# Kernel optimization log

Measured on AMD Instinct MI355X. Metric: run time of the kernel, lower is better.

## Reference

```python
import jax, jax.numpy as jnp
import numpy as np

DIM = 256
HEADS = 8
WIN = 8
HIDDEN = 1024
EPS = 1e-5

def _rel_pos_index(w):
    coords = np.stack(np.meshgrid(np.arange(w), np.arange(w), indexing='ij'))  # [2,w,w]
    cf = coords.reshape(2, -1)
    rel = cf[:, :, None] - cf[:, None, :]  # [2,N,N]
    rel = rel.transpose(1, 2, 0)
    rel[:, :, 0] += w - 1
    rel[:, :, 1] += w - 1
    rel[:, :, 0] *= 2 * w - 1
    return jnp.asarray(rel.sum(-1))  # [N,N] int

REL_IDX = _rel_pos_index(WIN)

def _layernorm(x, g, b):
    mu = jnp.mean(x, -1, keepdims=True)
    var = jnp.mean(jnp.square(x - mu), -1, keepdims=True)
    return (x - mu) * jax.lax.rsqrt(var + EPS) * g + b

def setup_inputs() -> dict:
    key = jax.random.key(0)
    ks = jax.random.split(key, 12)
    s = 0.02
    return {
        'x': jax.random.normal(ks[0], (16, 4096, 256), jnp.float32),
        'H': 64,
        'W': 64,
        'ln1_g': jnp.ones((DIM,), jnp.float32),
        'ln1_b': jnp.zeros((DIM,), jnp.float32),
        'qkv_w': jax.random.normal(ks[1], (DIM, 3 * DIM), jnp.float32) * s,
        'proj_w': jax.random.normal(ks[2], (DIM, DIM), jnp.float32) * s,
        'proj_b': jnp.zeros((DIM,), jnp.float32),
        'rel_bias_table': jax.random.normal(ks[3], ((2 * WIN - 1) ** 2, HEADS), jnp.float32) * s,
        'ln2_g': jnp.ones((DIM,), jnp.float32),
        'ln2_b': jnp.zeros((DIM,), jnp.float32),
        'fc1_w': jax.random.normal(ks[4], (DIM, HIDDEN), jnp.float32) * s,
        'fc1_b': jnp.zeros((HIDDEN,), jnp.float32),
        'fc2_w': jax.random.normal(ks[5], (HIDDEN, DIM), jnp.float32) * s,
        'fc2_b': jnp.zeros((DIM,), jnp.float32),
    }

def reference(x, H, W, ln1_g, ln1_b, qkv_w, proj_w, proj_b, rel_bias_table,
              ln2_g, ln2_b, fc1_w, fc1_b, fc2_w, fc2_b):
    B, L, C = x.shape
    w = WIN
    N = w * w
    head_dim = C // HEADS
    scale = head_dim ** -0.5

    shortcut = x
    h = _layernorm(x, ln1_g, ln1_b).reshape(B, H, W, C)
    # H, W chosen divisible by window_size -> pad_h = pad_w = 0 (faithful fast path)
    # window partition: [B*nW, N, C]
    h = h.reshape(B, H // w, w, W // w, w, C).transpose(0, 1, 3, 2, 4, 5)
    xw = h.reshape(-1, N, C)
    Bw = xw.shape[0]

    qkv = (xw @ qkv_w).reshape(Bw, N, 3, HEADS, head_dim)
    q = qkv[:, :, 0].transpose(0, 2, 1, 3) * scale  # [Bw,h,N,d]
    k = qkv[:, :, 1].transpose(0, 2, 1, 3)
    v = qkv[:, :, 2].transpose(0, 2, 1, 3)

    attn = jnp.einsum('bhnd,bhmd->bhnm', q, k)
    bias = rel_bias_table[REL_IDX.reshape(-1)].reshape(N, N, HEADS).transpose(2, 0, 1)
    attn = jax.nn.softmax(attn + bias[None], axis=-1)
    out = jnp.einsum('bhnm,bhmd->bhnd', attn, v).transpose(0, 2, 1, 3).reshape(Bw, N, C)
    out = out @ proj_w + proj_b

    # window reverse
    out = out.reshape(B, H // w, W // w, w, w, C).transpose(0, 1, 3, 2, 4, 5)
    out = out.reshape(B, L, C)

    x = shortcut + out
    h2 = _layernorm(x, ln2_g, ln2_b)
    mlp = jax.nn.gelu(h2 @ fc1_w + fc1_b, approximate=False) @ fc2_w + fc2_b
    return x + mlp
```

## Files before the change

### kernel.cpp

```cpp
#include <hip/hip_runtime.h>
#include <hip/hip_bf16.h>

typedef __attribute__((ext_vector_type(8))) short bf16x8;
typedef __attribute__((ext_vector_type(4))) float f32x4;

typedef __attribute__((address_space(3))) void LdsVoid;
typedef const __attribute__((address_space(1))) void GblVoid;

__device__ __forceinline__ void gload16(const void* g, void* l) {
  __builtin_amdgcn_global_load_lds((GblVoid*)g, (LdsVoid*)l, 16, 0, 0);
}

__device__ __forceinline__ unsigned short f2bf(float f) {
  union { float f; unsigned int u; } x; x.f = f;
  unsigned int r = (x.u + 0x7fffu + ((x.u >> 16) & 1u)) >> 16;
  return (unsigned short)r;
}

__device__ __forceinline__ unsigned int cvt_pk_bf16(float a, float b) {
  unsigned int r;
  asm("v_cvt_pk_bf16_f32 %0, %1, %2" : "=v"(r) : "v"(a), "v"(b));
  return r;
}

__device__ __forceinline__ float gelu_f(float t) {
  float u = t * (0.7978845608028654f + 0.03567740814f * t * t);
  float e = __expf(2.0f * u);
  float th = 1.0f - 2.0f * __builtin_amdgcn_rcpf(e + 1.0f);
  return 0.5f * t * (1.0f + th);
}

__global__ __launch_bounds__(256) void prep_w(
    const float* __restrict__ qw, const float* __restrict__ pw,
    const float* __restrict__ f1, const float* __restrict__ f2,
    unsigned short* __restrict__ out) {
  int idx = blockIdx.x * 256 + threadIdx.x;
  if (idx < 196608) { int n = idx >> 8, k = idx & 255; out[idx] = f2bf(qw[k * 768 + n]); return; }
  int i2 = idx - 196608;
  if (i2 < 65536) { int n = i2 >> 8, k = i2 & 255; out[idx] = f2bf(pw[k * 256 + n]); return; }
  int i3 = i2 - 65536;
  if (i3 < 262144) { int n = i3 >> 8, k = i3 & 255; out[idx] = f2bf(f1[k * 1024 + n]); return; }
  int i4 = i3 - 262144;
  { int n = i4 >> 10, k = i4 & 1023; out[idx] = f2bf(f2[k * 256 + n]); }
}

__global__ __launch_bounds__(256) void ln1_kernel(
    const float* __restrict__ x, const float* __restrict__ g, const float* __restrict__ b,
    unsigned short* __restrict__ xn) {
  int lane = threadIdx.x & 63, wid = threadIdx.x >> 6;
  size_t t = (size_t)blockIdx.x * 4 + wid;
  float4 v = ((const float4*)(x + t * 256))[lane];
  float s = v.x + v.y + v.z + v.w;
  #pragma unroll
  for (int m = 1; m < 64; m <<= 1) s += __shfl_xor(s, m);
  float mean = s * (1.0f / 256.0f);
  float dx = v.x - mean, dy = v.y - mean, dz = v.z - mean, dw = v.w - mean;
  float q = dx * dx + dy * dy + dz * dz + dw * dw;
  #pragma unroll
  for (int m = 1; m < 64; m <<= 1) q += __shfl_xor(q, m);
  float rstd = rsqrtf(q * (1.0f / 256.0f) + 1e-5f);
  float4 gg = ((const float4*)g)[lane];
  float4 bb = ((const float4*)b)[lane];
  unsigned int o0 = cvt_pk_bf16(dx * rstd * gg.x + bb.x, dy * rstd * gg.y + bb.y);
  unsigned int o1 = cvt_pk_bf16(dz * rstd * gg.z + bb.z, dw * rstd * gg.w + bb.w);
  int bI = (int)(t >> 12), rem = (int)t & 4095, y = rem >> 6, xc = rem & 63;
  size_t r = ((size_t)(bI * 64 + (y >> 3) * 8 + (xc >> 3))) * 64 + (y & 7) * 8 + (xc & 7);
  uint2 o; o.x = o0; o.y = o1;
  ((uint2*)(xn + r * 256))[lane] = o;
}

template <int EPI>
__global__ __launch_bounds__(512, 2) void gemm8p(
    const unsigned short* __restrict__ A, const unsigned short* __restrict__ Bt,
    unsigned short* __restrict__ outb, float* __restrict__ outf,
    const float* __restrict__ bias, const float* __restrict__ xres,
    int M, int N, int K) {
  extern __shared__ unsigned short lds[];
  const int tid = threadIdx.x;
  const int lane = tid & 63, w = tid >> 6;
  const int cl = lane & 15, cg = lane >> 4;
  const int wr = w >> 2, wc = w & 3;
  const unsigned nwg = gridDim.x * gridDim.y;
  const unsigned orig = blockIdx.y * gridDim.x + blockIdx.x;
  const unsigned virt = (orig & 7) * (nwg >> 3) + (orig >> 3);
  const unsigned bx = virt % gridDim.x, by = virt / gridDim.x;
  const size_t m0 = (size_t)by * 256, n0 = (size_t)bx * 256;
  const int nkt = K >> 6;

  const int trow = tid >> 3, tslot = tid & 7;
  const unsigned short* aSrc = A + (m0 + trow) * K + (tslot ^ (trow & 7)) * 8;
  const unsigned short* bSrc = Bt + (n0 + trow) * K + (tslot ^ (trow & 7)) * 8;

  const int slk0 = ((0 + cg) ^ (cl & 7)) * 8;
  const int slk1 = ((4 + cg) ^ (cl & 7)) * 8;

  f32x4 acc[8][4] = {};
  bf16x8 af[2][4], b0[2][2], b1[2][2];

  #define STAGE(ISB, KT, HALF)                                                    \
    { unsigned short* d_ = lds + (ISB) * 32768 + ((KT) & 1) * 16384 +             \
                           (HALF) * 8192 + tid * 8;                               \
      const unsigned short* s_ = ((ISB) ? bSrc : aSrc) +                          \
                                 (size_t)((HALF) * 128) * K + (KT) * 64;          \
      gload16(s_, d_); gload16(s_ + (size_t)64 * K, d_ + 4096); }

  #define READ_A(MH, P)                                                           \
    { const unsigned short* ba_ = lds + (P) * 16384 + (MH) * 8192 +               \
                                  (wr * 64 + cl) * 64;                            \
      _Pragma("unroll")                                                           \
      for (int mi = 0; mi < 4; ++mi) {                                            \
        af[0][mi] = *(const bf16x8*)(ba_ + mi * 1024 + slk0);                     \
        af[1][mi] = *(const bf16x8*)(ba_ + mi * 1024 + slk1); } }

  #define READ_B(NH, P, D)                                                        \
    { const unsigned short* bb_ = lds + 32768 + (P) * 16384 + (NH) * 8192 +       \
                                  (wc * 32 + cl) * 64;                            \
      _Pragma("unroll")                                                           \
      for (int ni = 0; ni < 2; ++ni) {                                            \
        D[0][ni] = *(const bf16x8*)(bb_ + ni * 1024 + slk0);                      \
        D[1][ni] = *(const bf16x8*)(bb_ + ni * 1024 + slk1); } }

  #define MFMA_Q(MH, NH, D)                                                       \
    { _Pragma("unroll")                                                           \
      for (int kk = 0; kk < 2; ++kk)                                              \
        _Pragma("unroll")                                                         \
        for (int mi = 0; mi < 4; ++mi)                                            \
          _Pragma("unroll")                                                       \
          for (int ni = 0; ni < 2; ++ni)                                          \
            acc[(MH) * 4 + mi][(NH) * 2 + ni] =                                   \
                __builtin_amdgcn_mfma_f32_16x16x32_bf16(                          \
                    D[kk][ni], af[kk][mi], acc[(MH) * 4 + mi][(NH) * 2 + ni],     \
                    0, 0, 0); }

  #define BAR() __builtin_amdgcn_s_barrier()
  #define LGKM0() { asm volatile("s_waitcnt lgkmcnt(0)" ::: "memory");            \
                    __builtin_amdgcn_sched_barrier(0); }

  STAGE(0, 0, 0); STAGE(1, 0, 1); STAGE(1, 0, 0); STAGE(0, 0, 1);
  STAGE(0, 1, 0); STAGE(1, 1, 1);
  asm volatile("s_waitcnt vmcnt(4)" ::: "memory");
  BAR();

  for (int kt = 0; kt < nkt; ++kt) {
    const int p = kt & 1;
    READ_A(0, p); READ_B(0, p, b0);
    if (kt + 1 < nkt) STAGE(1, kt + 1, 0);
    BAR(); LGKM0();
    __builtin_amdgcn_s_setprio(1); MFMA_Q(0, 0, b0); __builtin_amdgcn_s_setprio(0);
    BAR();
    READ_B(1, p, b1);
    if (kt + 1 < nkt) STAGE(0, kt + 1, 1);
    BAR(); LGKM0();
    __builtin_amdgcn_s_setprio(1); MFMA_Q(0, 1, b1); __builtin_amdgcn_s_setprio(0);
    BAR();
    READ_A(1, p);
    if (kt + 2 < nkt) STAGE(0, kt + 2, 0);
    BAR(); LGKM0();
    __builtin_amdgcn_s_setprio(1); MFMA_Q(1, 1, b1); __builtin_amdgcn_s_setprio(0);
    BAR();
    if (kt + 2 < nkt) STAGE(1, kt + 2, 1);
    BAR();
    __builtin_amdgcn_s_setprio(1); MFMA_Q(1, 0, b0); __builtin_amdgcn_s_setprio(0);
    if (kt + 2 < nkt) { asm volatile("s_waitcnt vmcnt(4)" ::: "memory"); }
    else              { asm volatile("s_waitcnt vmcnt(0)" ::: "memory"); }
    BAR();
  }
  #undef STAGE
  #undef READ_A
  #undef READ_B
  #undef MFMA_Q

  #pragma unroll
  for (int mi8 = 0; mi8 < 8; ++mi8) {
    const size_t row = m0 + (mi8 >> 2) * 128 + wr * 64 + (mi8 & 3) * 16 + cl;
    #pragma unroll
    for (int ni4 = 0; ni4 < 4; ++ni4) {
      const size_t col = n0 + (ni4 >> 1) * 128 + wc * 32 + (ni4 & 1) * 16 + cg * 4;
      f32x4 v = acc[mi8][ni4];
      if (EPI == 0) {
        uint2 o;
        o.x = cvt_pk_bf16(v[0], v[1]);
        o.y = cvt_pk_bf16(v[2], v[3]);
        *(uint2*)&outb[row * N + col] = o;
      } else if (EPI == 1) {
        float4 bb = *(const float4*)&bias[col];
        float g0 = gelu_f(v[0] + bb.x), g1 = gelu_f(v[1] + bb.y);
        float g2 = gelu_f(v[2] + bb.z), g3 = gelu_f(v[3] + bb.w);
        uint2 o;
        o.x = cvt_pk_bf16(g0, g1);
        o.y = cvt_pk_bf16(g2, g3);
        *(uint2*)&outb[row * N + col] = o;
      } else if (EPI == 3) {
        float4 bb = *(const float4*)&bias[col];
        float4* pp = (float4*)&outf[row * N + col];
        float4 old = *pp;
        old.x += v[0] + bb.x; old.y += v[1] + bb.y;
        old.z += v[2] + bb.z; old.w += v[3] + bb.w;
        *pp = old;
      } else if (EPI == 4) {
        int winr = (int)(row >> 6), pos = (int)(row & 63);
        int bI = winr >> 6, wy = (winr >> 3) & 7, wx = winr & 7;
        size_t tt = (size_t)bI * 4096 + (size_t)(wy * 8 + (pos >> 3)) * 64 + wx * 8 + (pos & 7);
        float4 bb = *(const float4*)&bias[col];
        float4 xr = *(const float4*)&xres[tt * 256 + col];
        float4 o;
        o.x = v[0] + bb.x + xr.x; o.y = v[1] + bb.y + xr.y;
        o.z = v[2] + bb.z + xr.z; o.w = v[3] + bb.w + xr.w;
        *(float4*)&outf[tt * 256 + col] = o;
      }
    }
  }
}

__global__ __launch_bounds__(256) void attn_win(
    const unsigned short* __restrict__ qkv, const float* __restrict__ table,
    unsigned short* __restrict__ out) {
  __shared__ float tbl[1800];
  __shared__ __align__(16) unsigned short p_lds[4][64 * 72];
  __shared__ __align__(16) unsigned short vt_lds[4][32 * 72];
  const int tid = threadIdx.x, lane = tid & 63, wid = tid >> 6;
  const int cl = lane & 15, cg = lane >> 4;
  for (int i = tid; i < 1800; i += 256) tbl[i] = table[i];
  __syncthreads();
  const size_t wbase = (size_t)blockIdx.x * 64;
  unsigned short* P = p_lds[wid];
  unsigned short* VT = vt_lds[wid];
  const float scale = 0.17677669529663687f;

  for (int hh = 0; hh < 2; ++hh) {
    const int h = wid + hh * 4;
    const int qoff = h * 32, koff = 256 + h * 32, voff = 512 + h * 32;
    bf16x8 qf[4], kf[4];
    #pragma unroll
    for (int mi = 0; mi < 4; ++mi)
      qf[mi] = *(const bf16x8*)&qkv[(wbase + mi * 16 + cl) * 768 + qoff + cg * 8];
    #pragma unroll
    for (int nj = 0; nj < 4; ++nj)
      kf[nj] = *(const bf16x8*)&qkv[(wbase + nj * 16 + cl) * 768 + koff + cg * 8];
    f32x4 S[4][4] = {};
    #pragma unroll
    for (int mi = 0; mi < 4; ++mi)
      #pragma unroll
      for (int nj = 0; nj < 4; ++nj)
        S[mi][nj] = __builtin_amdgcn_mfma_f32_16x16x32_bf16(qf[mi], kf[nj], S[mi][nj], 0, 0, 0);

    {
      const unsigned short* vrow = &qkv[(wbase + lane) * 768 + voff];
      unsigned short tmp[32];
      #pragma unroll
      for (int p = 0; p < 4; ++p) *(uint4*)&tmp[p * 8] = ((const uint4*)vrow)[p];
      #pragma unroll
      for (int d = 0; d < 32; ++d) VT[d * 72 + lane] = tmp[d];
    }

    #pragma unroll
    for (int mi = 0; mi < 4; ++mi) {
      #pragma unroll
      for (int r = 0; r < 4; ++r) {
        const int i = mi * 16 + cg * 4 + r;
        const int yi = i >> 3, xi = i & 7;
        float v[4];
        float m = -1e30f;
        #pragma unroll
        for (int nj = 0; nj < 4; ++nj) {
          const int j = nj * 16 + cl;
          const int yj = j >> 3, xj = j & 7;
          float bia = tbl[((yi - yj + 7) * 15 + (xi - xj + 7)) * 8 + h];
          v[nj] = S[mi][nj][r] * scale + bia;
          m = fmaxf(m, v[nj]);
        }
        #pragma unroll
        for (int mk = 1; mk < 16; mk <<= 1) m = fmaxf(m, __shfl_xor(m, mk));
        float s = 0.0f;
        #pragma unroll
        for (int nj = 0; nj < 4; ++nj) { v[nj] = __expf(v[nj] - m); s += v[nj]; }
        #pragma unroll
        for (int mk = 1; mk < 16; mk <<= 1) s += __shfl_xor(s, mk);
        const float rinv = __builtin_amdgcn_rcpf(s);
        #pragma unroll
        for (int nj = 0; nj < 4; ++nj) P[i * 72 + nj * 16 + cl] = f2bf(v[nj] * rinv);
      }
    }

    f32x4 O[4][2] = {};
    #pragma unroll
    for (int ks = 0; ks < 2; ++ks) {
      bf16x8 pa[4], vb[2];
      #pragma unroll
      for (int mi = 0; mi < 4; ++mi)
        pa[mi] = *(const bf16x8*)&P[(mi * 16 + cl) * 72 + ks * 32 + cg * 8];
      #pragma unroll
      for (int nd = 0; nd < 2; ++nd)
        vb[nd] = *(const bf16x8*)&VT[(nd * 16 + cl) * 72 + ks * 32 + cg * 8];
      #pragma unroll
      for (int mi = 0; mi < 4; ++mi)
        #pragma unroll
        for (int nd = 0; nd < 2; ++nd)
          O[mi][nd] = __builtin_amdgcn_mfma_f32_16x16x32_bf16(vb[nd], pa[mi], O[mi][nd], 0, 0, 0);
    }

    #pragma unroll
    for (int mi = 0; mi < 4; ++mi)
      #pragma unroll
      for (int nd = 0; nd < 2; ++nd) {
        uint2 o;
        o.x = cvt_pk_bf16(O[mi][nd][0], O[mi][nd][1]);
        o.y = cvt_pk_bf16(O[mi][nd][2], O[mi][nd][3]);
        *(uint2*)&out[(wbase + mi * 16 + cl) * 256 + h * 32 + nd * 16 + cg * 4] = o;
      }
  }
}

__global__ __launch_bounds__(256) void ln2_kernel(
    const float* __restrict__ x2, const float* __restrict__ g, const float* __restrict__ b,
    unsigned short* __restrict__ h2) {
  int lane = threadIdx.x & 63, wid = threadIdx.x >> 6;
  size_t t = (size_t)blockIdx.x * 4 + wid;
  float4 v = ((const float4*)(x2 + t * 256))[lane];
  float s = v.x + v.y + v.z + v.w;
  #pragma unroll
  for (int m = 1; m < 64; m <<= 1) s += __shfl_xor(s, m);
  float mean = s * (1.0f / 256.0f);
  float dx = v.x - mean, dy = v.y - mean, dz = v.z - mean, dw = v.w - mean;
  float q = dx * dx + dy * dy + dz * dz + dw * dw;
  #pragma unroll
  for (int m = 1; m < 64; m <<= 1) q += __shfl_xor(q, m);
  float rstd = rsqrtf(q * (1.0f / 256.0f) + 1e-5f);
  float4 gg = ((const float4*)g)[lane];
  float4 bb = ((const float4*)b)[lane];
  uint2 o;
  o.x = cvt_pk_bf16(dx * rstd * gg.x + bb.x, dy * rstd * gg.y + bb.y);
  o.y = cvt_pk_bf16(dz * rstd * gg.z + bb.z, dw * rstd * gg.w + bb.w);
  ((uint2*)(h2 + t * 256))[lane] = o;
}

extern "C" void kernel_launch(void* const* d_in, const int* in_sizes, int n_in,
                              void* d_out, int out_size, void* d_ws, size_t ws_size,
                              hipStream_t stream) {
  (void)in_sizes; (void)n_in; (void)out_size; (void)ws_size;
  const float* x       = (const float*)d_in[0];
  const float* ln1_g   = (const float*)d_in[3];
  const float* ln1_b   = (const float*)d_in[4];
  const float* qkv_w   = (const float*)d_in[5];
  const float* proj_w  = (const float*)d_in[6];
  const float* proj_b  = (const float*)d_in[7];
  const float* rel_tbl = (const float*)d_in[8];
  const float* ln2_g   = (const float*)d_in[9];
  const float* ln2_b   = (const float*)d_in[10];
  const float* fc1_w   = (const float*)d_in[11];
  const float* fc1_b   = (const float*)d_in[12];
  const float* fc2_w   = (const float*)d_in[13];
  const float* fc2_b   = (const float*)d_in[14];
  float* out = (float*)d_out;

  char* ws = (char*)d_ws;
  const size_t OFF_XN   = 1572864;
  const size_t OFF_QKV  = OFF_XN + 33554432;
  const size_t OFF_ATTN = OFF_QKV + 100663296;
  unsigned short* Wt      = (unsigned short*)ws;
  unsigned short* xn      = (unsigned short*)(ws + OFF_XN);
  unsigned short* h2      = xn;
  unsigned short* qkv     = (unsigned short*)(ws + OFF_QKV);
  unsigned short* fc1out  = (unsigned short*)(ws + OFF_QKV);
  unsigned short* attnout = (unsigned short*)(ws + OFF_ATTN);

  hipFuncSetAttribute((const void*)gemm8p<0>, hipFuncAttributeMaxDynamicSharedMemorySize, 131072);
  hipFuncSetAttribute((const void*)gemm8p<1>, hipFuncAttributeMaxDynamicSharedMemorySize, 131072);
  hipFuncSetAttribute((const void*)gemm8p<3>, hipFuncAttributeMaxDynamicSharedMemorySize, 131072);
  hipFuncSetAttribute((const void*)gemm8p<4>, hipFuncAttributeMaxDynamicSharedMemorySize, 131072);

  prep_w<<<3072, 256, 0, stream>>>(qkv_w, proj_w, fc1_w, fc2_w, Wt);
  ln1_kernel<<<16384, 256, 0, stream>>>(x, ln1_g, ln1_b, xn);
  gemm8p<0><<<dim3(3, 256), 512, 131072, stream>>>(xn, Wt, qkv, nullptr, nullptr, nullptr, 65536, 768, 256);
  attn_win<<<1024, 256, 0, stream>>>(qkv, rel_tbl, attnout);
  gemm8p<4><<<dim3(1, 256), 512, 131072, stream>>>(attnout, Wt + 196608, nullptr, out, proj_b, x, 65536, 256, 256);
  ln2_kernel<<<16384, 256, 0, stream>>>(out, ln2_g, ln2_b, h2);
  gemm8p<1><<<dim3(4, 256), 512, 131072, stream>>>(h2, Wt + 262144, fc1out, nullptr, fc1_b, nullptr, 65536, 1024, 256);
  gemm8p<3><<<dim3(1, 256), 512, 131072, stream>>>(fc1out, Wt + 524288, nullptr, out, fc2_b, nullptr, 65536, 256, 1024);
}
```

Before: 431.8 us.

## Fuse MLP fc1+GELU+fc2 into one kernel keeping hidden activations in LDS

Replaces the two MLP GEMM launches with a single kernel. Each 128-row block computes the fc1 output one 256-column chunk at a time, applies bias and GELU, and writes the chunk as bf16 into a swizzled LDS buffer. It then accumulates fc2 from that buffer, so the 65536x1024 hidden tensor never goes through global memory. The cost is that A and W fragments are loaded straight from global memory without LDS staging or pipelining, only 512 blocks are launched, and register pressure is high. Any of these could leave the MFMA units underfed compared with the tuned gemm8p path.

New measurement: 626.0 us. +45.0%, slower.

```diff
diff --git a/kernel.cpp b/kernel.cpp
--- a/kernel.cpp
+++ b/kernel.cpp
@@ -182,21 +182,6 @@
         o.x = cvt_pk_bf16(v[0], v[1]);
         o.y = cvt_pk_bf16(v[2], v[3]);
         *(uint2*)&outb[row * N + col] = o;
-      } else if (EPI == 1) {
-        float4 bb = *(const float4*)&bias[col];
-        float g0 = gelu_f(v[0] + bb.x), g1 = gelu_f(v[1] + bb.y);
-        float g2 = gelu_f(v[2] + bb.z), g3 = gelu_f(v[3] + bb.w);
-        uint2 o;
-        o.x = cvt_pk_bf16(g0, g1);
-        o.y = cvt_pk_bf16(g2, g3);
-        *(uint2*)&outb[row * N + col] = o;
-      } else if (EPI == 3) {
-        float4 bb = *(const float4*)&bias[col];
-        float4* pp = (float4*)&outf[row * N + col];
-        float4 old = *pp;
-        old.x += v[0] + bb.x; old.y += v[1] + bb.y;
-        old.z += v[2] + bb.z; old.w += v[3] + bb.w;
-        *pp = old;
       } else if (EPI == 4) {
         int winr = (int)(row >> 6), pos = (int)(row & 63);
         int bI = winr >> 6, wy = (winr >> 3) & 7, wx = winr & 7;
@@ -208,6 +193,89 @@
         o.z = v[2] + bb.z + xr.z; o.w = v[3] + bb.w + xr.w;
         *(float4*)&outf[tt * 256 + col] = o;
       }
+    }
+  }
+}
+
+__global__ __launch_bounds__(512, 2) void mlp_fused(
+    const unsigned short* __restrict__ h2,
+    const unsigned short* __restrict__ w1t,
+    const unsigned short* __restrict__ w2t,
+    const float* __restrict__ b1, const float* __restrict__ b2,
+    float* __restrict__ out) {
+  __shared__ __align__(16) unsigned short inter[128 * 256];
+  const int tid = threadIdx.x, lane = tid & 63, w = tid >> 6;
+  const int cl = lane & 15, cg = lane >> 4;
+  const int wr = w >> 2, wc = w & 3;
+  const size_t m0 = (size_t)blockIdx.x * 128;
+  const int rbase = wr * 64 + cl;
+
+  f32x4 acc2[4][4] = {};
+
+  for (int kc = 0; kc < 4; ++kc) {
+    f32x4 accA[4][4] = {};
+    #pragma unroll
+    for (int kk = 0; kk < 8; ++kk) {
+      bf16x8 a[4], wv[4];
+      #pragma unroll
+      for (int mi = 0; mi < 4; ++mi)
+        a[mi] = *(const bf16x8*)&h2[(m0 + rbase + mi * 16) * 256 + kk * 32 + cg * 8];
+      #pragma unroll
+      for (int ni = 0; ni < 4; ++ni)
+        wv[ni] = *(const bf16x8*)&w1t[(size_t)(kc * 256 + wc * 64 + ni * 16 + cl) * 256 + kk * 32 + cg * 8];
+      #pragma unroll
+      for (int mi = 0; mi < 4; ++mi)
+        #pragma unroll
+        for (int ni = 0; ni < 4; ++ni)
+          accA[mi][ni] = __builtin_amdgcn_mfma_f32_16x16x32_bf16(wv[ni], a[mi], accA[mi][ni], 0, 0, 0);
+    }
+    #pragma unroll
+    for (int mi = 0; mi < 4; ++mi) {
+      const int r = rbase + mi * 16;
+      #pragma unroll
+      for (int ni = 0; ni < 4; ++ni) {
+        const int icol = kc * 256 + wc * 64 + ni * 16 + cg * 4;
+        float4 bb = *(const float4*)&b1[icol];
+        float g0 = gelu_f(accA[mi][ni][0] + bb.x), g1 = gelu_f(accA[mi][ni][1] + bb.y);
+        float g2 = gelu_f(accA[mi][ni][2] + bb.z), g3 = gelu_f(accA[mi][ni][3] + bb.w);
+        uint2 o; o.x = cvt_pk_bf16(g0, g1); o.y = cvt_pk_bf16(g2, g3);
+        const int slot = wc * 8 + ni * 2 + (cg >> 1);
+        *(uint2*)(inter + r * 256 + ((slot ^ (r & 7)) << 3) + (cg & 1) * 4) = o;
+      }
+    }
+    __syncthreads();
+    #pragma unroll
+    for (int kk = 0; kk < 8; ++kk) {
+      bf16x8 aB[4], wv[4];
+      #pragma unroll
+      for (int mi = 0; mi < 4; ++mi) {
+        const int r = rbase + mi * 16;
+        aB[mi] = *(const bf16x8*)(inter + r * 256 + (((kk * 4 + cg) ^ (r & 7)) << 3));
+      }
+      #pragma unroll
+      for (int ni = 0; ni < 4; ++ni)
+        wv[ni] = *(const bf16x8*)&w2t[(size_t)(wc * 64 + ni * 16 + cl) * 1024 + kc * 256 + kk * 32 + cg * 8];
+      #pragma unroll
+      for (int mi = 0; mi < 4; ++mi)
+        #pragma unroll
+        for (int ni = 0; ni < 4; ++ni)
+          acc2[mi][ni] = __builtin_amdgcn_mfma_f32_16x16x32_bf16(wv[ni], aB[mi], acc2[mi][ni], 0, 0, 0);
+    }
+    __syncthreads();
+  }
+
+  #pragma unroll
+  for (int mi = 0; mi < 4; ++mi) {
+    const size_t row = m0 + rbase + mi * 16;
+    #pragma unroll
+    for (int ni = 0; ni < 4; ++ni) {
+      const int col = wc * 64 + ni * 16 + cg * 4;
+      float4 bb = *(const float4*)&b2[col];
+      float4* pp = (float4*)&out[row * 256 + col];
+      float4 old = *pp;
+      old.x += acc2[mi][ni][0] + bb.x; old.y += acc2[mi][ni][1] + bb.y;
+      old.z += acc2[mi][ni][2] + bb.z; old.w += acc2[mi][ni][3] + bb.w;
+      *pp = old;
     }
   }
 }
@@ -361,12 +429,9 @@
   unsigned short* xn      = (unsigned short*)(ws + OFF_XN);
   unsigned short* h2      = xn;
   unsigned short* qkv     = (unsigned short*)(ws + OFF_QKV);
-  unsigned short* fc1out  = (unsigned short*)(ws + OFF_QKV);
   unsigned short* attnout = (unsigned short*)(ws + OFF_ATTN);
 
   hipFuncSetAttribute((const void*)gemm8p<0>, hipFuncAttributeMaxDynamicSharedMemorySize, 131072);
-  hipFuncSetAttribute((const void*)gemm8p<1>, hipFuncAttributeMaxDynamicSharedMemorySize, 131072);
-  hipFuncSetAttribute((const void*)gemm8p<3>, hipFuncAttributeMaxDynamicSharedMemorySize, 131072);
   hipFuncSetAttribute((const void*)gemm8p<4>, hipFuncAttributeMaxDynamicSharedMemorySize, 131072);
 
   prep_w<<<3072, 256, 0, stream>>>(qkv_w, proj_w, fc1_w, fc2_w, Wt);
@@ -375,6 +440,5 @@
   attn_win<<<1024, 256, 0, stream>>>(qkv, rel_tbl, attnout);
   gemm8p<4><<<dim3(1, 256), 512, 131072, stream>>>(attnout, Wt + 196608, nullptr, out, proj_b, x, 65536, 256, 256);
   ln2_kernel<<<16384, 256, 0, stream>>>(out, ln2_g, ln2_b, h2);
-  gemm8p<1><<<dim3(4, 256), 512, 131072, stream>>>(h2, Wt + 262144, fc1out, nullptr, fc1_b, nullptr, 65536, 1024, 256);
-  gemm8p<3><<<dim3(1, 256), 512, 131072, stream>>>(fc1out, Wt + 524288, nullptr, out, fc2_b, nullptr, 65536, 256, 1024);
-}
+  mlp_fused<<<512, 512, 0, stream>>>(h2, Wt + 262144, Wt + 524288, fc1_b, fc2_b, out);
+}
```
